# Optimization experiments

Measured on AMD Instinct MI355X. Metric: run time of the kernel, lower is better.

The kernel has to match this reference:

```python
import jax
import jax.numpy as jnp
from jax import lax
import numpy as np

B, T, C, L = 512, 512, 128, 80
BLANK = C - 1  # Keras ctc_batch_cost uses last class as blank
NEG = -1e30
EPS = 1e-7


def setup_inputs() -> dict:
    key = jax.random.key(0)
    k1, k2 = jax.random.split(key)
    # y_pred: positive "probability-like" activations, as ctc_batch_cost expects
    y_pred = jax.random.uniform(k1, (B, T, C), dtype=jnp.float32)
    # labels: non-blank symbols in [0, C-2]
    y_true = jax.random.randint(k2, (B, L), 0, C - 1, dtype=jnp.int64)
    return {"y_true": y_true, "y_pred": y_pred}


def _ctc_loss(log_probs, labels):
    """log_probs: [B,T,C] log-softmax; labels: [B,L] ints. Returns [B,1] loss."""
    b, t, c = log_probs.shape
    l = labels.shape[1]
    s = 2 * l + 1
    # extended label sequence: blank, l1, blank, l2, ..., blank  -> [B,S]
    ext = jnp.full((b, s), BLANK, dtype=labels.dtype).at[:, 1::2].set(labels)
    # per-time log-prob of each extended symbol: [B,T,S]
    lp = jnp.take_along_axis(log_probs, ext[:, None, :], axis=2)
    # skip-transition allowed where symbol is non-blank and differs from s-2
    ext_m2 = jnp.concatenate([jnp.full((b, 2), BLANK, ext.dtype), ext[:, :-2]], axis=1)
    allow2 = (ext != BLANK) & (ext != ext_m2)  # [B,S]

    alpha0 = (jnp.full((b, s), NEG, dtype=log_probs.dtype)
              .at[:, 0].set(lp[:, 0, 0])
              .at[:, 1].set(lp[:, 0, 1]))

    neg1 = jnp.full((b, 1), NEG, dtype=log_probs.dtype)
    neg2 = jnp.full((b, 2), NEG, dtype=log_probs.dtype)

    def step(alpha, lp_t):
        a1 = jnp.concatenate([neg1, alpha[:, :-1]], axis=1)
        a2 = jnp.concatenate([neg2, alpha[:, :-2]], axis=1)
        a2 = jnp.where(allow2, a2, NEG)
        m = jnp.maximum(jnp.maximum(alpha, a1), a2)
        lse = m + jnp.log(jnp.exp(alpha - m) + jnp.exp(a1 - m) + jnp.exp(a2 - m))
        return lp_t + lse, None

    lp_t_first = jnp.swapaxes(lp, 0, 1)  # [T,B,S]
    alphaT, _ = lax.scan(step, alpha0, lp_t_first[1:])
    loss = -jnp.logaddexp(alphaT[:, s - 1], alphaT[:, s - 2])  # [B]
    return loss[:, None]


def reference(y_true, y_pred):
    # K.ctc_batch_cost: log(y_pred + eps), then tf.nn.ctc_loss (softmax inside)
    log_probs = jax.nn.log_softmax(jnp.log(y_pred + EPS), axis=-1)
    return _ctc_loss(log_probs, y_true)
```

## Files before the change

### kernel.cpp

```cpp
#include <hip/hip_runtime.h>

#define B_ 512
#define T_ 512
#define C_ 128
#define L_ 80
#define BLANK_ 127
#define EPS_ 1e-7f
#define LN2_ 0.6931471805599453f

#define LOG2F(x) __builtin_amdgcn_logf(x)

template <int CTRL>
__device__ __forceinline__ int dpp_i(int x) {
  return __builtin_amdgcn_update_dpp(0, x, CTRL, 0xF, 0xF, true);
}
template <int CTRL>
__device__ __forceinline__ float dpp_f(float x) {
  return __int_as_float(
      __builtin_amdgcn_update_dpp(0, __float_as_int(x), CTRL, 0xF, 0xF, true));
}
#define DPP_WSHR1 0x138
#define DPP_XOR1  0xB1
#define DPP_XOR2  0x4E
#define DPP_HMIRR 0x141
#define DPP_MIRR  0x140

__global__ __launch_bounds__(256) void ctc_fused(
    const int* __restrict__ labels,
    const float* __restrict__ y_pred,
    float* __restrict__ out)
{
  const int b = blockIdx.x, tid = threadIdx.x;
  const int wid = tid >> 6, lane = tid & 63;
  const float* gp = y_pred + (size_t)b * T_ * C_;

  __shared__ float comb[4];

  const bool evenLane = ((lane & 1) == 0);

  float A0 = 0.f, A1 = 0.f, A2 = 0.f;
  int E = 0;

  if (wid == 0) {
    auto labAt = [&](int k) -> int {
      return (k >= 0 && k < L_) ? labels[b * L_ + k] : BLANK_;
    };
    int ea, eb;
    float m0, m1, m2;
    if (evenLane) {
      const int k1 = (3 * lane) >> 1;
      ea = labAt(k1); eb = ea;
      m0 = 0.f; m2 = 0.f;
      m1 = ((k1 < L_) && (k1 == 0 || ea != labAt(k1 - 1))) ? 1.f : 0.f;
    } else {
      const int k0 = (3 * lane - 1) >> 1;
      const int k2 = k0 + 1;
      ea = labAt(k0); eb = labAt(k2);
      m0 = ((k0 < L_) && (k0 == 0 || ea != labAt(k0 - 1))) ? 1.f : 0.f;
      m1 = 0.f;
      m2 = ((k2 < L_) && (eb != ea)) ? 1.f : 0.f;
    }
    A0 = (lane == 0) ? 1.f : 0.f;

    const float* pea = gp + ea;
    const float* peb = gp + eb;
    const float* pbl = gp + BLANK_;

    float gaA[8], gbA[8], pbA[8];
    float gaB[8], gbB[8], pbB[8];
    float gaC[8], gbC[8], pbC[8];

    auto loadG = [&](float (&g)[8], float (&h)[8], float (&p)[8], int t0) {
      #pragma unroll
      for (int j = 0; j < 8; ++j) {
        g[j] = pea[(t0 + j) * C_];
        h[j] = peb[(t0 + j) * C_];
        p[j] = pbl[(t0 + j) * C_];
      }
    };
    auto stepG = [&](float (&g)[8], float (&h)[8], float (&p)[8]) {
      const int EL = dpp_i<DPP_WSHR1>(E);
      const int d = E - EL;
      #pragma unroll
      for (int j = 0; j < 8; ++j) {
        const float p1 = dpp_f<DPP_WSHR1>(A1);
        const float p2 = dpp_f<DPP_WSHR1>(A2);
        const float p1p = ldexpf(p1, d);
        const float p2p = ldexpf(p2, d);
        const float q0 = (evenLane ? p[j] : g[j]) + EPS_;
        const float q1 = (evenLane ? g[j] : p[j]) + EPS_;
        const float q2 = (evenLane ? p[j] : h[j]) + EPS_;
        const float t0 = q0 * fmaf(m0, p1p, A0 + p2p);
        const float t1 = q1 * fmaf(m1, p2p, A1 + A0);
        const float t2 = q2 * fmaf(m2, A0, A2 + A1);
        A0 = t0; A1 = t1; A2 = t2;
      }
      const float mx = fmaxf(fmaxf(A0, A1), A2);
      int ee = (int)((__float_as_uint(mx) >> 23) & 255u) - 127;
      const bool z = (mx == 0.f);
      ee = z ? 0 : ee;
      A0 = ldexpf(A0, -ee); A1 = ldexpf(A1, -ee); A2 = ldexpf(A2, -ee);
      E = z ? EL : (E - ee);
    };

    loadG(gaA, gbA, pbA, 0);
    loadG(gaB, gbB, pbB, 8);
    for (int g = 0; g < 63; g += 3) {
      loadG(gaC, gbC, pbC, 8 * (g + 2));
      stepG(gaA, gbA, pbA);
      loadG(gaA, gbA, pbA, 8 * (g + 3));
      stepG(gaB, gbB, pbB);
      if (g + 4 < 64) loadG(gaB, gbB, pbB, 8 * (g + 4));
      stepG(gaC, gbC, pbC);
    }
    stepG(gaA, gbA, pbA);
  } else {
    const int w = wid - 1;
    const int rgrp = lane >> 3, j16 = lane & 7;
    const int N = (64 - w + 2) / 3;
    float4 S0[4], S1[4], S2[4];
    float Sacc = 0.f;

    auto loadB = [&](float4 (&S)[4], int i) {
      const int blk = w + 3 * i;
      const float4* src =
          (const float4*)(gp + (size_t)(8 * blk + rgrp) * C_) + 4 * j16;
      #pragma unroll
      for (int k = 0; k < 4; ++k) S[k] = src[k];
    };
    auto sumB = [&](float4 (&S)[4]) {
      float s = 0.f;
      #pragma unroll
      for (int k = 0; k < 4; ++k) {
        float4 v = S[k];
        v.x += EPS_; v.y += EPS_; v.z += EPS_; v.w += EPS_;
        s += (v.x + v.y) + (v.z + v.w);
      }
      s += dpp_f<DPP_XOR1>(s);
      s += dpp_f<DPP_XOR2>(s);
      s += dpp_f<DPP_HMIRR>(s);
      Sacc += LOG2F(s);
    };

    loadB(S0, 0);
    if (1 < N) loadB(S1, 1);
    if (2 < N) loadB(S2, 2);
    for (int i = 0; i < N; i += 3) {
      sumB(S0); if (i + 3 < N) loadB(S0, i + 3);
      if (i + 1 < N) { sumB(S1); if (i + 4 < N) loadB(S1, i + 4); }
      if (i + 2 < N) { sumB(S2); if (i + 5 < N) loadB(S2, i + 5); }
    }

    float s = Sacc;
    s += dpp_f<DPP_XOR1>(s);
    s += dpp_f<DPP_XOR2>(s);
    s += dpp_f<DPP_HMIRR>(s);
    s += dpp_f<DPP_MIRR>(s);
    s += __shfl_xor(s, 16, 64);
    s += __shfl_xor(s, 32, 64);
    if (lane == 0) comb[wid] = s * 0.125f;
  }

  __syncthreads();

  if (wid == 0 && lane == 53) {
    const float Stot = comb[1] + comb[2] + comb[3];
    out[b] = LN2_ * (Stot - (LOG2F(A0 + A1) - (float)E));
  }
}

extern "C" void kernel_launch(void* const* d_in, const int* in_sizes, int n_in,
                              void* d_out, int out_size, void* d_ws, size_t ws_size,
                              hipStream_t stream) {
  const int*   labels = (const int*)d_in[0];
  const float* y_pred = (const float*)d_in[1];
  float*       out    = (float*)d_out;
  ctc_fused<<<dim3(B_), dim3(256), 0, stream>>>(labels, y_pred, out);
}
```

Measured before the change: 212.3 us.

## Stream y_pred through LDS ring buffer from producer warps to recurrence warp

New measurement: 194.0 us. 1.09x faster.

```diff
diff --git a/kernel.cpp b/kernel.cpp
--- a/kernel.cpp
+++ b/kernel.cpp
@@ -7,6 +7,7 @@
 #define BLANK_ 127
 #define EPS_ 1e-7f
 #define LN2_ 0.6931471805599453f
+#define RING_ 16
 
 #define LOG2F(x) __builtin_amdgcn_logf(x)
 
@@ -34,12 +35,16 @@
   const int wid = tid >> 6, lane = tid & 63;
   const float* gp = y_pred + (size_t)b * T_ * C_;
 
+  __shared__ float ring[RING_ * 1024];
+  __shared__ int   flags[64];
+  __shared__ int   cons;
   __shared__ float comb[4];
 
+  if (tid < 64) flags[tid] = 0;
+  if (tid == 0) cons = 0;
+  __syncthreads();
+
   const bool evenLane = ((lane & 1) == 0);
-
-  float A0 = 0.f, A1 = 0.f, A2 = 0.f;
-  int E = 0;
 
   if (wid == 0) {
     auto labAt = [&](int k) -> int {
@@ -60,22 +65,26 @@
       m1 = 0.f;
       m2 = ((k2 < L_) && (eb != ea)) ? 1.f : 0.f;
     }
-    A0 = (lane == 0) ? 1.f : 0.f;
-
-    const float* pea = gp + ea;
-    const float* peb = gp + eb;
-    const float* pbl = gp + BLANK_;
-
-    float gaA[8], gbA[8], pbA[8];
-    float gaB[8], gbB[8], pbB[8];
-    float gaC[8], gbC[8], pbC[8];
-
-    auto loadG = [&](float (&g)[8], float (&h)[8], float (&p)[8], int t0) {
+    float A0 = (lane == 0) ? 1.f : 0.f, A1 = 0.f, A2 = 0.f;
+    int E = 0;
+
+    auto waitFlag = [&](int i) {
+      while (__hip_atomic_load(&flags[i], __ATOMIC_ACQUIRE,
+                               __HIP_MEMORY_SCOPE_WORKGROUP) == 0)
+        __builtin_amdgcn_s_sleep(2);
+    };
+    auto consSet = [&](int v) {
+      if (lane == 0)
+        __hip_atomic_store(&cons, v, __ATOMIC_RELAXED,
+                           __HIP_MEMORY_SCOPE_WORKGROUP);
+    };
+    auto gath = [&](float (&g)[8], float (&h)[8], float (&p)[8], int i) {
+      const float* rs = ring + (i & (RING_ - 1)) * 1024;
       #pragma unroll
       for (int j = 0; j < 8; ++j) {
-        g[j] = pea[(t0 + j) * C_];
-        h[j] = peb[(t0 + j) * C_];
-        p[j] = pbl[(t0 + j) * C_];
+        g[j] = rs[j * C_ + ea];
+        h[j] = rs[j * C_ + eb];
+        p[j] = rs[j * C_ + BLANK_];
       }
     };
     auto stepG = [&](float (&g)[8], float (&h)[8], float (&p)[8]) {
@@ -87,9 +96,9 @@
         const float p2 = dpp_f<DPP_WSHR1>(A2);
         const float p1p = ldexpf(p1, d);
         const float p2p = ldexpf(p2, d);
-        const float q0 = (evenLane ? p[j] : g[j]) + EPS_;
-        const float q1 = (evenLane ? g[j] : p[j]) + EPS_;
-        const float q2 = (evenLane ? p[j] : h[j]) + EPS_;
+        const float q0 = evenLane ? p[j] : g[j];
+        const float q1 = evenLane ? g[j] : p[j];
+        const float q2 = evenLane ? p[j] : h[j];
         const float t0 = q0 * fmaf(m0, p1p, A0 + p2p);
         const float t1 = q1 * fmaf(m1, p2p, A1 + A0);
         const float t2 = q2 * fmaf(m2, A0, A2 + A1);
@@ -103,52 +112,75 @@
       E = z ? EL : (E - ee);
     };
 
-    loadG(gaA, gbA, pbA, 0);
-    loadG(gaB, gbB, pbB, 8);
-    for (int g = 0; g < 63; g += 3) {
-      loadG(gaC, gbC, pbC, 8 * (g + 2));
+    float gaA[8], gbA[8], pbA[8], gaB[8], gbB[8], pbB[8];
+    waitFlag(0); gath(gaA, gbA, pbA, 0);
+    for (int i = 0; i < 64; i += 2) {
+      waitFlag(i + 1); gath(gaB, gbB, pbB, i + 1);
       stepG(gaA, gbA, pbA);
-      loadG(gaA, gbA, pbA, 8 * (g + 3));
+      consSet(i + 1);
+      if (i + 2 < 64) { waitFlag(i + 2); gath(gaA, gbA, pbA, i + 2); }
       stepG(gaB, gbB, pbB);
-      if (g + 4 < 64) loadG(gaB, gbB, pbB, 8 * (g + 4));
-      stepG(gaC, gbC, pbC);
-    }
-    stepG(gaA, gbA, pbA);
+      consSet(i + 2);
+    }
+
+    __syncthreads();
+
+    if (lane == 53) {
+      const float Stot = comb[1] + comb[2] + comb[3];
+      out[b] = LN2_ * (Stot - (LOG2F(A0 + A1) - (float)E));
+    }
   } else {
     const int w = wid - 1;
     const int rgrp = lane >> 3, j16 = lane & 7;
-    const int N = (64 - w + 2) / 3;
-    float4 S0[4], S1[4], S2[4];
+    float4 S0[4], S1[4];
     float Sacc = 0.f;
 
-    auto loadB = [&](float4 (&S)[4], int i) {
-      const int blk = w + 3 * i;
+    auto loadB = [&](float4 (&S)[4], int blk) {
       const float4* src =
           (const float4*)(gp + (size_t)(8 * blk + rgrp) * C_) + 4 * j16;
       #pragma unroll
       for (int k = 0; k < 4; ++k) S[k] = src[k];
     };
-    auto sumB = [&](float4 (&S)[4]) {
+    auto waitSlot = [&](int j) {
+      if (j >= RING_) {
+        while (__hip_atomic_load(&cons, __ATOMIC_RELAXED,
+                                 __HIP_MEMORY_SCOPE_WORKGROUP) < j - (RING_ - 1))
+          __builtin_amdgcn_s_sleep(8);
+      }
+    };
+    auto proc = [&](float4 (&S)[4], int j) {
+      float* slot = ring + (j & (RING_ - 1)) * 1024;
+      float4* wd = (float4*)(slot + rgrp * C_ + 16 * j16);
       float s = 0.f;
       #pragma unroll
       for (int k = 0; k < 4; ++k) {
         float4 v = S[k];
         v.x += EPS_; v.y += EPS_; v.z += EPS_; v.w += EPS_;
+        wd[k] = v;
         s += (v.x + v.y) + (v.z + v.w);
       }
       s += dpp_f<DPP_XOR1>(s);
       s += dpp_f<DPP_XOR2>(s);
       s += dpp_f<DPP_HMIRR>(s);
       Sacc += LOG2F(s);
-    };
-
-    loadB(S0, 0);
-    if (1 < N) loadB(S1, 1);
-    if (2 < N) loadB(S2, 2);
-    for (int i = 0; i < N; i += 3) {
-      sumB(S0); if (i + 3 < N) loadB(S0, i + 3);
-      if (i + 1 < N) { sumB(S1); if (i + 4 < N) loadB(S1, i + 4); }
-      if (i + 2 < N) { sumB(S2); if (i + 5 < N) loadB(S2, i + 5); }
+      asm volatile("s_waitcnt lgkmcnt(0)" ::: "memory");
+      if (lane == 0)
+        __hip_atomic_store(&flags[j], 1, __ATOMIC_RELEASE,
+                           __HIP_MEMORY_SCOPE_WORKGROUP);
+    };
+
+    int j = w;
+    loadB(S0, j);
+    if (j + 3 < 64) loadB(S1, j + 3);
+    while (true) {
+      waitSlot(j); proc(S0, j);
+      if (j + 6 < 64) loadB(S0, j + 6);
+      j += 3;
+      if (j >= 64) break;
+      waitSlot(j); proc(S1, j);
+      if (j + 6 < 64) loadB(S1, j + 6);
+      j += 3;
+      if (j >= 64) break;
     }
 
     float s = Sacc;
@@ -159,13 +191,8 @@
     s += __shfl_xor(s, 16, 64);
     s += __shfl_xor(s, 32, 64);
     if (lane == 0) comb[wid] = s * 0.125f;
-  }
-
-  __syncthreads();
-
-  if (wid == 0 && lane == 53) {
-    const float Stot = comb[1] + comb[2] + comb[3];
-    out[b] = LN2_ * (Stot - (LOG2F(A0 + A1) - (float)E));
+
+    __syncthreads();
   }
 }
 
```
